# Optimization experiments

Hardware: AMD Instinct MI355X
Metric: run time of the kernel (lower is better)

The kernel has to match this reference:

```python
import jax, jax.numpy as jnp
import numpy as np

PARTS = [list(range(0, 17)), list(range(17, 22)), list(range(22, 27)),
         list(range(27, 36)), list(range(36, 42)), list(range(42, 48)),
         list(range(48, 68))]
NUM_PARTS = len(PARTS)
V_JOINTS = max(max(p) for p in PARTS) + 1  # 68
# joint -> part index (same as get_corr_joints)
JOINTS = np.zeros((V_JOINTS,), dtype=np.int32)
for j, part in enumerate(PARTS):
    for i in part:
        JOINTS[i] = j
BN_EPS = 1e-5


def setup_inputs() -> dict:
    key = jax.random.key(0)
    k0, k1, k2 = jax.random.split(key, 3)
    N, C, T, V = 512, 1024, 1, V_JOINTS
    x = jax.random.normal(k0, (N, C, T, V), dtype=jnp.float32)
    conv1_w = jax.random.normal(k1, (C // 4, C), dtype=jnp.float32) * 0.02  # 1x1 conv C->C/4
    conv1_b = jnp.zeros((C // 4,), dtype=jnp.float32)
    conv2_w = jax.random.normal(k2, (2,), dtype=jnp.float32) * 0.5  # 1x1 conv 2->1
    conv2_b = jnp.zeros((), dtype=jnp.float32)
    bn_gamma = jnp.ones((C,), dtype=jnp.float32)
    bn_beta = jnp.zeros((C,), dtype=jnp.float32)
    return {"x": x, "conv1_w": conv1_w, "conv1_b": conv1_b,
            "conv2_w": conv2_w, "conv2_b": conv2_b,
            "bn_gamma": bn_gamma, "bn_beta": bn_beta}


def _forward(x, conv1_w, conv1_b, conv2_w, conv2_b, bn_gamma, bn_beta):
    N, C, T, V = x.shape  # T must be 1 (required by original .view)
    joints = jnp.asarray(JOINTS)
    P = NUM_PARTS
    # part-wise mean pool over joints: (V,P) normalized one-hot
    M = jax.nn.one_hot(joints, P, dtype=x.dtype)
    M = M / jnp.sum(M, axis=0, keepdims=True)
    x_parts = jnp.einsum('nctv,vp->nctp', x, M)            # (N,C,T,P)
    # conv1: 1x1, C -> C/4
    h = jnp.einsum('nctp,oc->notp', x_parts, conv1_w) + conv1_b[None, :, None, None]
    x_cap = jnp.mean(h, axis=1, keepdims=True)             # channel avg pool
    x_cmp = jnp.max(h, axis=1, keepdims=True)              # channel max pool
    # conv2: 1x1, 2 -> 1 (cat order is (avg, max))
    att = conv2_w[0] * x_cap + conv2_w[1] * x_cmp + conv2_b  # (N,1,T,P)
    att = jnp.broadcast_to(att, (N, C, T, P)).reshape(N, C, P)
    att = jax.nn.softmax(att, axis=-1)                     # softmax over parts
    # scatter part attention back to joints
    att_j = att[:, :, joints][:, :, None, :]               # (N,C,1,V)
    y = x * att_j
    # BatchNorm2d (training mode: batch stats over N,T,V per channel)
    mean = jnp.mean(y, axis=(0, 2, 3), keepdims=True)
    var = jnp.var(y, axis=(0, 2, 3), keepdims=True)
    y_bn = (y - mean) * jax.lax.rsqrt(var + BN_EPS)
    y_bn = y_bn * bn_gamma[None, :, None, None] + bn_beta[None, :, None, None]
    return jax.nn.relu(y_bn + x)


def reference(x, conv1_w, conv1_b, conv2_w, conv2_b, bn_gamma, bn_beta):
    return _forward(x, conv1_w, conv1_b, conv2_w, conv2_b, bn_gamma, bn_beta)
```

## Files before the change

kernel.cpp:

```cpp
#include <hip/hip_runtime.h>

#define NN 512
#define CC 1024
#define OO 256
#define VV 68
#define PP 7
#define NC (NN*CC)
#define NV_CNT 34816.0f

typedef float floatx4 __attribute__((ext_vector_type(4)));

__device__ __forceinline__ int part_of(int v){
  return (v>=17)+(v>=22)+(v>=27)+(v>=36)+(v>=42)+(v>=48);
}

__global__ __launch_bounds__(256) void k0_prep(const float* __restrict__ w1,
    float* __restrict__ w1p){
  int g = blockIdx.x*256 + threadIdx.x;
  int o = g >> 8, cb = g & 255;
  float4 v = ((const float4*)w1)[g];
  ((float4*)w1p)[cb*256 + o] = v;
}

__global__ __launch_bounds__(256) void k1_partsum(const float* __restrict__ x,
    float* __restrict__ S, float* __restrict__ S2){
  __shared__ float stg[68*129];
  int R = blockIdx.x*128;
  const float4* src = (const float4*)(x + (size_t)R*VV);
  #pragma unroll
  for (int k=0;k<9;k++){
    int g = k*256 + threadIdx.x;
    if (k==8 && threadIdx.x>=128) break;
    float4 v4 = src[g];
    int row = g/17, q = g - row*17;
    stg[(q*4+0)*129 + row] = v4.x;
    stg[(q*4+1)*129 + row] = v4.y;
    stg[(q*4+2)*129 + row] = v4.z;
    stg[(q*4+3)*129 + row] = v4.w;
  }
  __syncthreads();

  int row  = threadIdx.x & 127;
  int half = threadIdx.x >> 7;
  float s[PP], q2[PP];
  #pragma unroll
  for (int p=0;p<PP;p++){ s[p]=0.f; q2[p]=0.f; }
  if (half==0){
    #pragma unroll
    for (int v=0; v<34; v++){
      int p = part_of(v);
      float e = stg[v*129 + row];
      s[p] += e;
      q2[p] = fmaf(e, e, q2[p]);
    }
  } else {
    #pragma unroll
    for (int v=34; v<68; v++){
      int p = part_of(v);
      float e = stg[v*129 + row];
      s[p] += e;
      q2[p] = fmaf(e, e, q2[p]);
    }
  }
  __syncthreads();
  float* hs = stg;
  float* hq = stg + 128*PP;
  if (half==1){
    #pragma unroll
    for (int p=0;p<PP;p++){ hs[row*PP+p]=s[p]; hq[row*PP+p]=q2[p]; }
  }
  __syncthreads();
  if (half==0){
    int r = R + row;
    #pragma unroll
    for (int p=0;p<PP;p++){
      S [p*NC + r] = s[p]  + hs[row*PP+p];
      S2[p*NC + r] = q2[p] + hq[row*PP+p];
    }
  }
}

__global__ __launch_bounds__(256) void k2_att(const float* __restrict__ S,
    const float* __restrict__ S2, const float* __restrict__ w1p,
    const float* __restrict__ b1, const float* __restrict__ w2,
    const float* __restrict__ b2, float* __restrict__ att,
    float* __restrict__ partial){
  int n = blockIdx.x;
  int t = threadIdx.x;

  __shared__ float4 sSf4[PP*256];
  __shared__ float hred[2048];
  __shared__ float red_s[4][PP], red_m[4][PP], pre[PP], att_s[PP];
  float* sSl = (float*)sSf4;

  for (int u = t; u < PP*256; u += 256){
    int p = u >> 8, cb = u & 255;
    sSf4[u] = *(const float4*)(S + (size_t)p*NC + (size_t)n*CC + cb*4);
  }
  __syncthreads();

  int oh = t & 31, ch = t >> 5;
  float acc[8][PP];
  #pragma unroll
  for (int k=0;k<8;k++)
    #pragma unroll
    for (int p=0;p<PP;p++) acc[k][p] = 0.f;

  const float4* wp = (const float4*)w1p;
  for (int i=0;i<32;i++){
    int gcb = ch*32 + i;
    const float4* wrow = wp + (size_t)gcb*256 + oh;
    float4 w[8];
    #pragma unroll
    for (int k=0;k<8;k++) w[k] = wrow[32*k];
    #pragma unroll
    for (int p=0;p<PP;p++){
      float4 sv = sSf4[p*256 + gcb];
      #pragma unroll
      for (int k=0;k<8;k++){
        acc[k][p] = fmaf(w[k].x, sv.x, acc[k][p]);
        acc[k][p] = fmaf(w[k].y, sv.y, acc[k][p]);
        acc[k][p] = fmaf(w[k].z, sv.z, acc[k][p]);
        acc[k][p] = fmaf(w[k].w, sv.w, acc[k][p]);
      }
    }
  }

  const float inv_cnt[PP] = {1.f/17.f,1.f/5.f,1.f/5.f,1.f/9.f,1.f/6.f,1.f/6.f,1.f/20.f};
  float bo = b1[t];
  float h[PP];
  #pragma unroll
  for (int p=0;p<PP;p++){
    __syncthreads();
    #pragma unroll
    for (int k=0;k<8;k++) hred[ch*256 + k*32 + oh] = acc[k][p];
    __syncthreads();
    float hs = 0.f;
    #pragma unroll
    for (int c8=0;c8<8;c8++) hs += hred[c8*256 + t];
    h[p] = fmaf(hs, inv_cnt[p], bo);
  }

  int lane = t & 63, wid = t >> 6;
  #pragma unroll
  for (int p=0;p<PP;p++){
    float sm = h[p], mx = h[p];
    #pragma unroll
    for (int off=32; off>0; off>>=1){
      sm += __shfl_down(sm, off, 64);
      mx = fmaxf(mx, __shfl_down(mx, off, 64));
    }
    if (lane==0){ red_s[wid][p]=sm; red_m[wid][p]=mx; }
  }
  __syncthreads();
  if (t < PP){
    int p = t;
    float sm = red_s[0][p]+red_s[1][p]+red_s[2][p]+red_s[3][p];
    float mx = fmaxf(fmaxf(red_m[0][p],red_m[1][p]),
                     fmaxf(red_m[2][p],red_m[3][p]));
    pre[p] = w2[0]*(sm*(1.f/(float)OO)) + w2[1]*mx + b2[0];
  }
  __syncthreads();
  if (t == 0){
    float m = pre[0];
    #pragma unroll
    for (int p=1;p<PP;p++) m = fmaxf(m, pre[p]);
    float e[PP], sum=0.f;
    #pragma unroll
    for (int p=0;p<PP;p++){ e[p] = expf(pre[p]-m); sum += e[p]; }
    float inv = 1.f/sum;
    #pragma unroll
    for (int p=0;p<PP;p++){
      float a = e[p]*inv;
      att_s[p] = a;
      att[n*PP+p] = a;
    }
  }
  __syncthreads();

  float a[PP], a2[PP];
  #pragma unroll
  for (int p=0;p<PP;p++){ a[p] = att_s[p]; a2[p] = a[p]*a[p]; }
  const float* S2n = S2 + (size_t)n*CC;
  #pragma unroll
  for (int j=0;j<4;j++){
    int c = j*256 + t;
    float sm=0.f, sq=0.f;
    #pragma unroll
    for (int p=0;p<PP;p++){
      sm = fmaf(a[p],  sSl[p*1024 + c],   sm);
      sq = fmaf(a2[p], S2n[(size_t)p*NC + c], sq);
    }
    partial[n*2048 + c]        = sm;
    partial[n*2048 + 1024 + c] = sq;
  }
}

__global__ __launch_bounds__(256) void k3b_finalize(const float* __restrict__ partial,
    const float* __restrict__ gamma, const float* __restrict__ beta,
    float* __restrict__ scsh){
  __shared__ float rs[8][32], rq[8][32];
  int cl = threadIdx.x & 31, grp = threadIdx.x >> 5;
  int c = blockIdx.x*32 + cl;
  float sm=0.f, sq=0.f;
  for (int i=0;i<64;i++){
    int n = grp*64 + i;
    sm += partial[n*2048 + c];
    sq += partial[n*2048 + 1024 + c];
  }
  rs[grp][cl] = sm; rq[grp][cl] = sq;
  __syncthreads();
  if (threadIdx.x < 32){
    float tsm=0.f, tsq=0.f;
    #pragma unroll
    for (int g=0; g<8; g++){ tsm += rs[g][threadIdx.x]; tsq += rq[g][threadIdx.x]; }
    int cc = blockIdx.x*32 + threadIdx.x;
    float mean = tsm * (1.0f/NV_CNT);
    float var  = tsq * (1.0f/NV_CNT) - mean*mean;
    float rstd = rsqrtf(var + 1e-5f);
    float sc = gamma[cc]*rstd;
    scsh[cc]        = sc;
    scsh[1024 + cc] = beta[cc] - mean*sc;
  }
}

__global__ __launch_bounds__(256) void k4_out(const float* __restrict__ x,
    const float* __restrict__ att, const float* __restrict__ scsh,
    float* __restrict__ out){
  int f = blockIdx.x*256 + threadIdx.x;
  int n = blockIdx.x / 68;
  __shared__ float s_att[PP];
  if (threadIdx.x < PP) s_att[threadIdx.x] = att[n*PP + threadIdx.x];
  __syncthreads();
  int r = f/17;
  int q = f - r*17;
  int v0 = q*4;
  int c = r & (CC-1);
  float4 xv = ((const float4*)x)[f];
  float sc = scsh[c];
  float sh = scsh[1024 + c];
  float vals[4];
  #pragma unroll
  for (int j=0;j<4;j++){
    int p = part_of(v0 + j);
    float a = s_att[p];
    float e = (j==0)?xv.x:(j==1)?xv.y:(j==2)?xv.z:xv.w;
    vals[j] = fmaxf(fmaf(e, fmaf(a, sc, 1.0f), sh), 0.0f);
  }
  floatx4 ov; ov.x=vals[0]; ov.y=vals[1]; ov.z=vals[2]; ov.w=vals[3];
  __builtin_nontemporal_store(ov, ((floatx4*)out) + f);
}

extern "C" void kernel_launch(void* const* d_in, const int* in_sizes, int n_in,
                              void* d_out, int out_size, void* d_ws, size_t ws_size,
                              hipStream_t stream) {
  const float* x     = (const float*)d_in[0];
  const float* w1    = (const float*)d_in[1];
  const float* b1    = (const float*)d_in[2];
  const float* w2    = (const float*)d_in[3];
  const float* b2    = (const float*)d_in[4];
  const float* gamma = (const float*)d_in[5];
  const float* beta  = (const float*)d_in[6];
  float* out = (float*)d_out;

  float* w1p     = (float*)d_ws;
  float* S       = w1p + OO*CC;
  float* S2      = S + 7*NC;
  float* partial = S2 + 7*NC;
  float* scsh    = partial + NN*2048;
  float* att     = scsh + 2048;

  k0_prep     <<<256,         256, 0, stream>>>(w1, w1p);
  k1_partsum  <<<NC/128,      256, 0, stream>>>(x, S, S2);
  k2_att      <<<NN,          256, 0, stream>>>(S, S2, w1p, b1, w2, b2, att, partial);
  k3b_finalize<<<32,          256, 0, stream>>>(partial, gamma, beta, scsh);
  k4_out      <<<(NC*17)/256, 256, 0, stream>>>(x, att, scsh, out);
}
```

Before: 326.0 us.

## Fuse part-sum pass into attention kernel, keeping per-part sums on chip

Merges the part-wise sum/sum-of-squares kernel into the attention kernel. Each block now loads its sample's full x slice (1024x68) in 8 chunks, reduces it into shared-memory part sums, and keeps the squared sums in registers. This removes the global S/S2 intermediates (7*NC floats each) and one launch. The cost is that only 512 blocks now stream x, each with a large shared-memory footprint, which may lower occupancy and memory-level parallelism during the read phase.

```diff
diff --git a/kernel.cpp b/kernel.cpp
--- a/kernel.cpp
+++ b/kernel.cpp
@@ -22,82 +22,70 @@
   ((float4*)w1p)[cb*256 + o] = v;
 }
 
-__global__ __launch_bounds__(256) void k1_partsum(const float* __restrict__ x,
-    float* __restrict__ S, float* __restrict__ S2){
-  __shared__ float stg[68*129];
-  int R = blockIdx.x*128;
-  const float4* src = (const float4*)(x + (size_t)R*VV);
-  #pragma unroll
-  for (int k=0;k<9;k++){
-    int g = k*256 + threadIdx.x;
-    if (k==8 && threadIdx.x>=128) break;
-    float4 v4 = src[g];
-    int row = g/17, q = g - row*17;
-    stg[(q*4+0)*129 + row] = v4.x;
-    stg[(q*4+1)*129 + row] = v4.y;
-    stg[(q*4+2)*129 + row] = v4.z;
-    stg[(q*4+3)*129 + row] = v4.w;
-  }
-  __syncthreads();
-
-  int row  = threadIdx.x & 127;
-  int half = threadIdx.x >> 7;
-  float s[PP], q2[PP];
-  #pragma unroll
-  for (int p=0;p<PP;p++){ s[p]=0.f; q2[p]=0.f; }
-  if (half==0){
-    #pragma unroll
-    for (int v=0; v<34; v++){
-      int p = part_of(v);
-      float e = stg[v*129 + row];
-      s[p] += e;
-      q2[p] = fmaf(e, e, q2[p]);
-    }
-  } else {
-    #pragma unroll
-    for (int v=34; v<68; v++){
-      int p = part_of(v);
-      float e = stg[v*129 + row];
-      s[p] += e;
-      q2[p] = fmaf(e, e, q2[p]);
-    }
-  }
-  __syncthreads();
-  float* hs = stg;
-  float* hq = stg + 128*PP;
-  if (half==1){
-    #pragma unroll
-    for (int p=0;p<PP;p++){ hs[row*PP+p]=s[p]; hq[row*PP+p]=q2[p]; }
-  }
-  __syncthreads();
-  if (half==0){
-    int r = R + row;
-    #pragma unroll
-    for (int p=0;p<PP;p++){
-      S [p*NC + r] = s[p]  + hs[row*PP+p];
-      S2[p*NC + r] = q2[p] + hq[row*PP+p];
-    }
-  }
-}
-
-__global__ __launch_bounds__(256) void k2_att(const float* __restrict__ S,
-    const float* __restrict__ S2, const float* __restrict__ w1p,
-    const float* __restrict__ b1, const float* __restrict__ w2,
-    const float* __restrict__ b2, float* __restrict__ att,
-    float* __restrict__ partial){
+__global__ __launch_bounds__(256) void k12_att(const float* __restrict__ x,
+    const float* __restrict__ w1p, const float* __restrict__ b1,
+    const float* __restrict__ w2, const float* __restrict__ b2,
+    float* __restrict__ att, float* __restrict__ partial){
   int n = blockIdx.x;
   int t = threadIdx.x;
 
+  __shared__ float stg[68*129];
   __shared__ float4 sSf4[PP*256];
-  __shared__ float hred[2048];
   __shared__ float red_s[4][PP], red_m[4][PP], pre[PP], att_s[PP];
-  float* sSl = (float*)sSf4;
-
-  for (int u = t; u < PP*256; u += 256){
-    int p = u >> 8, cb = u & 255;
-    sSf4[u] = *(const float4*)(S + (size_t)p*NC + (size_t)n*CC + cb*4);
-  }
-  __syncthreads();
+  float* sSl  = (float*)sSf4;
+  float* hred = stg;
+  float* sqt  = stg + 2048;
+
+  int row  = t & 127;
+  int half = t >> 7;
+
+  float q2r[8][4];
+  #pragma unroll
+  for (int j=0;j<8;j++){
+    q2r[j][0]=0.f; q2r[j][1]=0.f; q2r[j][2]=0.f; q2r[j][3]=0.f;
+  }
+
+  const float4* xb = (const float4*)(x + (size_t)n*CC*VV);
+  #pragma unroll
+  for (int j=0;j<8;j++){
+    const float4* src = xb + j*2176;
+    #pragma unroll
+    for (int k=0;k<9;k++){
+      int g = k*256 + t;
+      if (k==8 && t>=128) break;
+      float4 v4 = src[g];
+      int rr = g/17, q = g - rr*17;
+      stg[(q*4+0)*129 + rr] = v4.x;
+      stg[(q*4+1)*129 + rr] = v4.y;
+      stg[(q*4+2)*129 + rr] = v4.z;
+      stg[(q*4+3)*129 + rr] = v4.w;
+    }
+    __syncthreads();
+    if (half==0){
+      float s[3] = {0.f,0.f,0.f};
+      #pragma unroll
+      for (int v=0; v<27; v++){
+        int p = part_of(v);
+        float e = stg[v*129 + row];
+        s[p] += e;
+        q2r[j][p] = fmaf(e, e, q2r[j][p]);
+      }
+      #pragma unroll
+      for (int p=0;p<3;p++) sSl[p*1024 + j*128 + row] = s[p];
+    } else {
+      float s[4] = {0.f,0.f,0.f,0.f};
+      #pragma unroll
+      for (int v=27; v<68; v++){
+        int p = part_of(v) - 3;
+        float e = stg[v*129 + row];
+        s[p] += e;
+        q2r[j][p] = fmaf(e, e, q2r[j][p]);
+      }
+      #pragma unroll
+      for (int p=0;p<4;p++) sSl[(p+3)*1024 + j*128 + row] = s[p];
+    }
+    __syncthreads();
+  }
 
   int oh = t & 31, ch = t >> 5;
   float acc[8][PP];
@@ -178,21 +166,43 @@
   }
   __syncthreads();
 
-  float a[PP], a2[PP];
-  #pragma unroll
-  for (int p=0;p<PP;p++){ a[p] = att_s[p]; a2[p] = a[p]*a[p]; }
-  const float* S2n = S2 + (size_t)n*CC;
-  #pragma unroll
-  for (int j=0;j<4;j++){
-    int c = j*256 + t;
-    float sm=0.f, sq=0.f;
-    #pragma unroll
-    for (int p=0;p<PP;p++){
-      sm = fmaf(a[p],  sSl[p*1024 + c],   sm);
-      sq = fmaf(a2[p], S2n[(size_t)p*NC + c], sq);
-    }
-    partial[n*2048 + c]        = sm;
-    partial[n*2048 + 1024 + c] = sq;
+  float a[PP];
+  #pragma unroll
+  for (int p=0;p<PP;p++) a[p] = att_s[p];
+
+  #pragma unroll
+  for (int jj=0;jj<4;jj++){
+    int c = jj*256 + t;
+    float sm = 0.f;
+    #pragma unroll
+    for (int p=0;p<PP;p++) sm = fmaf(a[p], sSl[p*1024 + c], sm);
+    partial[n*2048 + c] = sm;
+  }
+
+  if (half==1){
+    #pragma unroll
+    for (int j=0;j<8;j++){
+      float sq = 0.f;
+      #pragma unroll
+      for (int p=0;p<4;p++){
+        float ap = a[p+3];
+        sq = fmaf(ap*ap, q2r[j][p], sq);
+      }
+      sqt[j*128 + row] = sq;
+    }
+  }
+  __syncthreads();
+  if (half==0){
+    #pragma unroll
+    for (int j=0;j<8;j++){
+      float sq = sqt[j*128 + row];
+      #pragma unroll
+      for (int p=0;p<3;p++){
+        float ap = a[p];
+        sq = fmaf(ap*ap, q2r[j][p], sq);
+      }
+      partial[n*2048 + 1024 + j*128 + row] = sq;
+    }
   }
 }
 
@@ -264,15 +274,12 @@
   float* out = (float*)d_out;
 
   float* w1p     = (float*)d_ws;
-  float* S       = w1p + OO*CC;
-  float* S2      = S + 7*NC;
-  float* partial = S2 + 7*NC;
+  float* partial = w1p + OO*CC;
   float* scsh    = partial + NN*2048;
   float* att     = scsh + 2048;
 
   k0_prep     <<<256,         256, 0, stream>>>(w1, w1p);
-  k1_partsum  <<<NC/128,      256, 0, stream>>>(x, S, S2);
-  k2_att      <<<NN,          256, 0, stream>>>(S, S2, w1p, b1, w2, b2, att, partial);
+  k12_att     <<<NN,          256, 0, stream>>>(x, w1p, b1, w2, b2, att, partial);
   k3b_finalize<<<32,          256, 0, stream>>>(partial, gamma, beta, scsh);
   k4_out      <<<(NC*17)/256, 256, 0, stream>>>(x, att, scsh, out);
 }
```

New measurement: 315.0 us. 3.4% less time.

## Replace per-sample attention GEMM with a shared-memory tiled GEMM and split kernels

Applied to the files above, without the earlier changes.

The per-sample attention kernel, in which every block streamed the whole transposed conv1 weight, is split into three kernels. A 32x32 shared-memory tiled GEMM computes part features times conv1 weights across all samples and parts. A softmax kernel and a separate BN-partial kernel follow. The weight pre-transpose kernel is removed, and the GEMM output buffer is aliased with the partial-sum buffer. This is meant to cut the repeated L2 weight traffic, at the cost of two extra launches and an extra round trip of the intermediate through global memory.

```diff
diff --git a/kernel.cpp b/kernel.cpp
--- a/kernel.cpp
+++ b/kernel.cpp
@@ -6,6 +6,7 @@
 #define VV 68
 #define PP 7
 #define NC (NN*CC)
+#define MM (PP*NN)
 #define NV_CNT 34816.0f
 
 typedef float floatx4 __attribute__((ext_vector_type(4)));
@@ -14,13 +15,6 @@
   return (v>=17)+(v>=22)+(v>=27)+(v>=36)+(v>=42)+(v>=48);
 }
 
-__global__ __launch_bounds__(256) void k0_prep(const float* __restrict__ w1,
-    float* __restrict__ w1p){
-  int g = blockIdx.x*256 + threadIdx.x;
-  int o = g >> 8, cb = g & 255;
-  float4 v = ((const float4*)w1)[g];
-  ((float4*)w1p)[cb*256 + o] = v;
-}
 
 __global__ __launch_bounds__(256) void k1_partsum(const float* __restrict__ x,
     float* __restrict__ S, float* __restrict__ S2){
@@ -80,71 +74,79 @@
   }
 }
 
-__global__ __launch_bounds__(256) void k2_att(const float* __restrict__ S,
-    const float* __restrict__ S2, const float* __restrict__ w1p,
+__global__ __launch_bounds__(256) void k2_gemm(const float* __restrict__ S,
+    const float* __restrict__ w1, float* __restrict__ h){
+  __shared__ float As[64][34];
+  __shared__ float Bs[64][34];
+  int b  = blockIdx.x;
+  int bm = b & 127 ? b % 112 : b % 112;
+  bm = b % 112;
+  int bo = b / 112;
+  int m0 = bm*32, o0 = bo*32;
+  int t  = threadIdx.x;
+  int to = t & 15, tm = t >> 4;
+  float acc00=0.f, acc01=0.f, acc10=0.f, acc11=0.f;
+
+  const float4* S4 = (const float4*)S;
+  const float4* W4 = (const float4*)w1;
+  for (int cc=0; cc<1024; cc+=64){
+    int ccg = cc >> 2;
+    #pragma unroll
+    for (int it=0; it<2; ++it){
+      int ml = it*16 + (t>>4);
+      int kg = t & 15;
+      float4 v = S4[(size_t)(m0+ml)*256 + ccg + kg];
+      As[kg*4+0][ml] = v.x;
+      As[kg*4+1][ml] = v.y;
+      As[kg*4+2][ml] = v.z;
+      As[kg*4+3][ml] = v.w;
+    }
+    #pragma unroll
+    for (int it=0; it<2; ++it){
+      int ol = it*16 + (t>>4);
+      int kg = t & 15;
+      float4 v = W4[(size_t)(o0+ol)*256 + ccg + kg];
+      Bs[kg*4+0][ol] = v.x;
+      Bs[kg*4+1][ol] = v.y;
+      Bs[kg*4+2][ol] = v.z;
+      Bs[kg*4+3][ol] = v.w;
+    }
+    __syncthreads();
+    #pragma unroll
+    for (int kk=0; kk<64; ++kk){
+      float2 av = *(const float2*)&As[kk][tm*2];
+      float2 bv = *(const float2*)&Bs[kk][to*2];
+      acc00 = fmaf(av.x, bv.x, acc00);
+      acc01 = fmaf(av.x, bv.y, acc01);
+      acc10 = fmaf(av.y, bv.x, acc10);
+      acc11 = fmaf(av.y, bv.y, acc11);
+    }
+    __syncthreads();
+  }
+  float2 r0; r0.x = acc00; r0.y = acc01;
+  float2 r1; r1.x = acc10; r1.y = acc11;
+  *(float2*)(h + (size_t)(m0 + tm*2    )*256 + o0 + to*2) = r0;
+  *(float2*)(h + (size_t)(m0 + tm*2 + 1)*256 + o0 + to*2) = r1;
+}
+
+__global__ __launch_bounds__(256) void k3_soft(const float* __restrict__ h,
     const float* __restrict__ b1, const float* __restrict__ w2,
-    const float* __restrict__ b2, float* __restrict__ att,
-    float* __restrict__ partial){
+    const float* __restrict__ b2, float* __restrict__ att){
   int n = blockIdx.x;
   int t = threadIdx.x;
-
-  __shared__ float4 sSf4[PP*256];
-  __shared__ float hred[2048];
-  __shared__ float red_s[4][PP], red_m[4][PP], pre[PP], att_s[PP];
-  float* sSl = (float*)sSf4;
-
-  for (int u = t; u < PP*256; u += 256){
-    int p = u >> 8, cb = u & 255;
-    sSf4[u] = *(const float4*)(S + (size_t)p*NC + (size_t)n*CC + cb*4);
-  }
-  __syncthreads();
-
-  int oh = t & 31, ch = t >> 5;
-  float acc[8][PP];
-  #pragma unroll
-  for (int k=0;k<8;k++)
-    #pragma unroll
-    for (int p=0;p<PP;p++) acc[k][p] = 0.f;
-
-  const float4* wp = (const float4*)w1p;
-  for (int i=0;i<32;i++){
-    int gcb = ch*32 + i;
-    const float4* wrow = wp + (size_t)gcb*256 + oh;
-    float4 w[8];
-    #pragma unroll
-    for (int k=0;k<8;k++) w[k] = wrow[32*k];
-    #pragma unroll
-    for (int p=0;p<PP;p++){
-      float4 sv = sSf4[p*256 + gcb];
-      #pragma unroll
-      for (int k=0;k<8;k++){
-        acc[k][p] = fmaf(w[k].x, sv.x, acc[k][p]);
-        acc[k][p] = fmaf(w[k].y, sv.y, acc[k][p]);
-        acc[k][p] = fmaf(w[k].z, sv.z, acc[k][p]);
-        acc[k][p] = fmaf(w[k].w, sv.w, acc[k][p]);
-      }
-    }
-  }
-
+  __shared__ float red_s[4][PP], red_m[4][PP], pre[PP];
   const float inv_cnt[PP] = {1.f/17.f,1.f/5.f,1.f/5.f,1.f/9.f,1.f/6.f,1.f/6.f,1.f/20.f};
   float bo = b1[t];
-  float h[PP];
+  float hv[PP];
   #pragma unroll
   for (int p=0;p<PP;p++){
-    __syncthreads();
-    #pragma unroll
-    for (int k=0;k<8;k++) hred[ch*256 + k*32 + oh] = acc[k][p];
-    __syncthreads();
-    float hs = 0.f;
-    #pragma unroll
-    for (int c8=0;c8<8;c8++) hs += hred[c8*256 + t];
-    h[p] = fmaf(hs, inv_cnt[p], bo);
-  }
-
+    float raw = h[(size_t)(p*NN + n)*256 + t];
+    hv[p] = fmaf(raw, inv_cnt[p], bo);
+  }
   int lane = t & 63, wid = t >> 6;
   #pragma unroll
   for (int p=0;p<PP;p++){
-    float sm = h[p], mx = h[p];
+    float sm = hv[p], mx = hv[p];
     #pragma unroll
     for (int off=32; off>0; off>>=1){
       sm += __shfl_down(sm, off, 64);
@@ -170,30 +172,29 @@
     for (int p=0;p<PP;p++){ e[p] = expf(pre[p]-m); sum += e[p]; }
     float inv = 1.f/sum;
     #pragma unroll
-    for (int p=0;p<PP;p++){
-      float a = e[p]*inv;
-      att_s[p] = a;
-      att[n*PP+p] = a;
-    }
-  }
-  __syncthreads();
-
-  float a[PP], a2[PP];
-  #pragma unroll
-  for (int p=0;p<PP;p++){ a[p] = att_s[p]; a2[p] = a[p]*a[p]; }
-  const float* S2n = S2 + (size_t)n*CC;
-  #pragma unroll
-  for (int j=0;j<4;j++){
-    int c = j*256 + t;
-    float sm=0.f, sq=0.f;
-    #pragma unroll
-    for (int p=0;p<PP;p++){
-      sm = fmaf(a[p],  sSl[p*1024 + c],   sm);
-      sq = fmaf(a2[p], S2n[(size_t)p*NC + c], sq);
-    }
-    partial[n*2048 + c]        = sm;
-    partial[n*2048 + 1024 + c] = sq;
-  }
+    for (int p=0;p<PP;p++) att[n*PP+p] = e[p]*inv;
+  }
+}
+
+__global__ __launch_bounds__(256) void k4_partial(const float* __restrict__ S,
+    const float* __restrict__ S2, const float* __restrict__ att,
+    float* __restrict__ partial){
+  int r = blockIdx.x*256 + threadIdx.x;
+  int n = r >> 10, c = r & 1023;
+  __shared__ float sa[PP], sa2[PP];
+  if (threadIdx.x < PP){
+    float a = att[n*PP + threadIdx.x];
+    sa[threadIdx.x] = a; sa2[threadIdx.x] = a*a;
+  }
+  __syncthreads();
+  float sm=0.f, sq=0.f;
+  #pragma unroll
+  for (int p=0;p<PP;p++){
+    sm = fmaf(sa[p],  S [(size_t)p*NC + r], sm);
+    sq = fmaf(sa2[p], S2[(size_t)p*NC + r], sq);
+  }
+  partial[n*2048 + c]        = sm;
+  partial[n*2048 + 1024 + c] = sq;
 }
 
 __global__ __launch_bounds__(256) void k3b_finalize(const float* __restrict__ partial,
@@ -263,16 +264,17 @@
   const float* beta  = (const float*)d_in[6];
   float* out = (float*)d_out;
 
-  float* w1p     = (float*)d_ws;
-  float* S       = w1p + OO*CC;
+  float* S       = (float*)d_ws;
   float* S2      = S + 7*NC;
-  float* partial = S2 + 7*NC;
-  float* scsh    = partial + NN*2048;
+  float* h       = S2 + 7*NC;
+  float* partial = h;
+  float* scsh    = h + NN*2048;
   float* att     = scsh + 2048;
 
-  k0_prep     <<<256,         256, 0, stream>>>(w1, w1p);
   k1_partsum  <<<NC/128,      256, 0, stream>>>(x, S, S2);
-  k2_att      <<<NN,          256, 0, stream>>>(S, S2, w1p, b1, w2, b2, att, partial);
+  k2_gemm     <<<(MM/32)*(OO/32), 256, 0, stream>>>(S, w1, h);
+  k3_soft     <<<NN,          256, 0, stream>>>(h, b1, w2, b2, att);
+  k4_partial  <<<NC/256,      256, 0, stream>>>(S, S2, att, partial);
   k3b_finalize<<<32,          256, 0, stream>>>(partial, gamma, beta, scsh);
   k4_out      <<<(NC*17)/256, 256, 0, stream>>>(x, att, scsh, out);
 }
```

New measurement: 373.3 us. 14.5% more time.
